# Optimization experiments

Measured on AMD Instinct MI355X. Metric: run time of the kernel, lower is better.

Reference implementation:

```python
import jax, jax.numpy as jnp
import numpy as np

H = 128        # hidden_channels
R = 32         # num_rbf
L = 2          # num_layers
CUTOFF = 4.5   # cutoff_upper (cutoff_lower = 0)
N_ATOMS = 2048
N_EDGES = 32768


def _tensor_norm(t):
    # Frobenius norm squared over the trailing 3x3 -> [N, H]
    return jnp.sum(t * t, axis=(-2, -1))


def _decompose(t):
    # Split into isotropic (I), antisymmetric (A), traceless symmetric (S) parts.
    eye = jnp.eye(3, dtype=t.dtype)
    I = (jnp.trace(t, axis1=-2, axis2=-1) / 3.0)[..., None, None] * eye
    A = 0.5 * (t - jnp.swapaxes(t, -2, -1))
    S = 0.5 * (t + jnp.swapaxes(t, -2, -1)) - I
    return I, A, S


def _chan_mix(T, W):
    # torch nn.Linear(H, H, bias=False) applied on the channel axis of [N,H,3,3]
    return jnp.einsum('nhij,gh->ngij', T, W)


def _interaction(X, edge_index, edge_weight, edge_attr, q,
                 W1, b1, W2, b2, W3, b3, Wt):
    N = X.shape[0]
    src, dst = edge_index[0], edge_index[1]
    # cosine cutoff (cutoff_lower = 0)
    C = 0.5 * (jnp.cos(edge_weight * (jnp.pi / CUTOFF)) + 1.0)
    C = C * (edge_weight < CUTOFF).astype(C.dtype)
    # edge scalar MLP: R -> H -> 2H -> 3H, silu
    ea = jax.nn.silu(edge_attr @ W1.T + b1)
    ea = jax.nn.silu(ea @ W2.T + b2)
    ea = jax.nn.silu(ea @ W3.T + b3)
    ea = (ea * C[:, None]).reshape(-1, H, 3)       # [E, H, 3]
    # normalize node tensors
    X = X / (_tensor_norm(X) + 1.0)[..., None, None]
    I, A, S = _decompose(X)
    I = _chan_mix(I, Wt[0])
    A = _chan_mix(A, Wt[1])
    S = _chan_mix(S, Wt[2])
    Y = I + A + S
    # per-edge tensor messages (Im + Am + Sm fused before the scatter)
    msg = (ea[:, :, 0, None, None] * I[dst]
           + ea[:, :, 1, None, None] * A[dst]
           + ea[:, :, 2, None, None] * S[dst])   # [E, H, 3, 3]
    M = jax.ops.segment_sum(msg, src, num_segments=N)
    # O(3) group: symmetrized tensor product, scaled by charge factor
    AB = jnp.matmul(M, Y) + jnp.matmul(Y, M)
    I, A, S = _decompose((1.0 + 0.1 * q[:, None, None, None]) * AB)
    normp1 = (_tensor_norm(I + A + S) + 1.0)[..., None, None]
    I, A, S = I / normp1, A / normp1, S / normp1
    I = _chan_mix(I, Wt[3])
    A = _chan_mix(A, Wt[4])
    S = _chan_mix(S, Wt[5])
    dX = I + A + S
    return X + dX + (1.0 + 0.1 * q[:, None, None, None]) * jnp.matmul(dX, dX)


def setup_inputs() -> dict:
    key = jax.random.key(0)
    ks = jax.random.split(key, 10)
    N, E = N_ATOMS, N_EDGES
    X = jax.random.normal(ks[0], (N, H, 3, 3), jnp.float32)
    edge_index = jax.random.randint(ks[1], (2, E), 0, N, jnp.int32)
    edge_weight = jax.random.uniform(ks[2], (E,), jnp.float32, 0.1, CUTOFF)
    edge_attr = jax.random.normal(ks[3], (E, R), jnp.float32)
    q = jax.random.normal(ks[4], (N,), jnp.float32) * 0.1
    s = 0.05
    Ws1 = jax.random.normal(ks[5], (L, H, R), jnp.float32) * s
    bs1 = jnp.zeros((L, H), jnp.float32)
    Ws2 = jax.random.normal(ks[6], (L, 2 * H, H), jnp.float32) * s
    bs2 = jnp.zeros((L, 2 * H), jnp.float32)
    Ws3 = jax.random.normal(ks[7], (L, 3 * H, 2 * H), jnp.float32) * s
    bs3 = jnp.zeros((L, 3 * H), jnp.float32)
    Wt = jax.random.normal(ks[8], (L, 6, H, H), jnp.float32) * s
    return dict(X=X, edge_attr=edge_attr, edge_weight=edge_weight, q=q,
                Ws1=Ws1, bs1=bs1, Ws2=Ws2, bs2=bs2, Ws3=Ws3, bs3=bs3,
                Wt=Wt, edge_index=edge_index)


def reference(X, edge_attr, edge_weight, q, Ws1, bs1, Ws2, bs2, Ws3, bs3, Wt, edge_index):
    for l in range(L):
        X = _interaction(X, edge_index, edge_weight, edge_attr, q,
                         Ws1[l], bs1[l], Ws2[l], bs2[l], Ws3[l], bs3[l], Wt[l])
    return X
```

## Files before the change

### kernel.cpp

```cpp
#include <hip/hip_runtime.h>
#include <hip/hip_bf16.h>
#include <math.h>

#define H 128
#define R 32
#define NATOMS 2048
#define NEDGES 32768
#define NH (NATOMS * H)
#define NP 1152
#define CUTOFF_F 4.5f
#define PI_OVER_CUTOFF 0.6981317007977318f

typedef __bf16 bf16x8 __attribute__((ext_vector_type(8)));
typedef float f32x4 __attribute__((ext_vector_type(4)));
typedef short short8 __attribute__((ext_vector_type(8)));
typedef unsigned short u16x4 __attribute__((ext_vector_type(4)));

#define BAR_LGKM() do { \
    asm volatile("s_waitcnt lgkmcnt(0)" ::: "memory"); \
    __builtin_amdgcn_s_barrier(); \
    asm volatile("" ::: "memory"); \
} while (0)

__device__ __forceinline__ float silu_f(float x) {
    return x / (1.f + __expf(-x));
}
__device__ __forceinline__ float b2f(unsigned short u) {
    return __uint_as_float(((unsigned)u) << 16);
}
__device__ __forceinline__ unsigned short f2b(float f) {
    __hip_bfloat16 h = __float2bfloat16(f);
    return __builtin_bit_cast(unsigned short, h);
}

__device__ __forceinline__ void build_full(const float d[9], float m[9]) {
    float i0 = d[0], a01 = d[1], a02 = d[2], a12 = d[3];
    float s00 = d[4], s01 = d[5], s02 = d[6], s11 = d[7], s12 = d[8];
    float s22 = -(s00 + s11);
    m[0] = i0 + s00;  m[1] = a01 + s01;  m[2] = a02 + s02;
    m[3] = s01 - a01; m[4] = i0 + s11;   m[5] = a12 + s12;
    m[6] = s02 - a02; m[7] = s12 - a12;  m[8] = i0 + s22;
}

#define C0 (NEDGES * R)
#define C1 (2 * H * R)
#define C2 (2 * 2 * H * H)
#define C3 (2 * 3 * H * 2 * H)
#define C4 (2 * 6 * H * H)
#define C5 2048
#define CAST_TOTAL (C0 + C1 + C2 + C3 + C4 + C5 + NH)
__global__ __launch_bounds__(256) void k_cast_all(
        const float* __restrict__ ea, const float* __restrict__ w1,
        const float* __restrict__ w2, const float* __restrict__ w3,
        const float* __restrict__ wt,
        __hip_bfloat16* __restrict__ oea, __hip_bfloat16* __restrict__ ow1,
        __hip_bfloat16* __restrict__ ow2, __hip_bfloat16* __restrict__ ow3,
        __hip_bfloat16* __restrict__ owt, int* __restrict__ cnt,
        const float* __restrict__ X, float* __restrict__ Xn,
        __hip_bfloat16* __restrict__ Db) {
    int i = blockIdx.x * 256 + threadIdx.x;
    if (i < C0) { oea[i] = __float2bfloat16(ea[i]); return; }
    i -= C0;
    if (i < C1) { ow1[i] = __float2bfloat16(w1[i]); return; }
    i -= C1;
    if (i < C2) { ow2[i] = __float2bfloat16(w2[i]); return; }
    i -= C2;
    if (i < C3) { ow3[i] = __float2bfloat16(w3[i]); return; }
    i -= C3;
    if (i < C4) { owt[i] = __float2bfloat16(wt[i]); return; }
    i -= C4;
    if (i < C5) { cnt[i] = 0; return; }
    i -= C5;
    if (i < NH) {
        const float* x = X + (size_t)i * 9;
        float v[9];
        float ss = 0.f;
#pragma unroll
        for (int j = 0; j < 9; j++) { v[j] = x[j]; ss += v[j] * v[j]; }
        float inv = 1.f / (ss + 1.f);
#pragma unroll
        for (int j = 0; j < 9; j++) { v[j] *= inv; Xn[(size_t)i * 9 + j] = v[j]; }
        float i0 = (v[0] + v[4] + v[8]) * (1.f / 3.f);
        unsigned short* D = (unsigned short*)Db + (size_t)(i >> 7) * NP + (i & 127);
        D[0 * H] = f2b(i0);
        D[1 * H] = f2b(0.5f * (v[1] - v[3]));
        D[2 * H] = f2b(0.5f * (v[2] - v[6]));
        D[3 * H] = f2b(0.5f * (v[5] - v[7]));
        D[4 * H] = f2b(v[0] - i0);
        D[5 * H] = f2b(0.5f * (v[1] + v[3]));
        D[6 * H] = f2b(0.5f * (v[2] + v[6]));
        D[7 * H] = f2b(v[4] - i0);
        D[8 * H] = f2b(0.5f * (v[5] + v[7]));
    }
}

struct TGm {
    static constexpr int BKm = 64;
    static constexpr int RB  = 128;
    static constexpr int SWZ = 7;
    static constexpr int NIT = 2;
    static constexpr int ABYTES = 128 * RB;
    static constexpr int BBYTES = 64 * RB;
    static constexpr int AISS = ABYTES / 4096;
    static constexpr int BISS = BBYTES / 4096;
    static constexpr int LDSB = ABYTES + BBYTES;
};

__device__ __forceinline__ void tile_gemm_mix(
        const __hip_bfloat16* __restrict__ A, int strideA,
        const __hip_bfloat16* __restrict__ W,
        int m0, int n0, char* lds, f32x4 acc[4][2]) {
    using T = TGm;
    const int t = threadIdx.x;
    const int lane = t & 63;
    const int w = t >> 6;

    auto stage = [&](int b, int it) {
        const int k0 = it * T::BKm;
        char* As = lds + b * T::LDSB;
        char* Bs = As + T::ABYTES;
#pragma unroll
        for (int i = 0; i < T::AISS; i++) {
            int base = (w * T::AISS + i) * 1024;
            int lin = base + lane * 16;
            int row = lin / T::RB;
            int slot = (lin % T::RB) >> 4;
            int sl = slot ^ (row & T::SWZ);
            const char* src = (const char*)(A + (size_t)(m0 + row) * strideA + k0) + sl * 16;
            __builtin_amdgcn_global_load_lds(
                (const __attribute__((address_space(1))) void*)src,
                (__attribute__((address_space(3))) void*)(As + base), 16, 0, 0);
        }
#pragma unroll
        for (int i = 0; i < T::BISS; i++) {
            int base = (w * T::BISS + i) * 1024;
            int lin = base + lane * 16;
            int row = lin / T::RB;
            int slot = (lin % T::RB) >> 4;
            int sl = slot ^ (row & T::SWZ);
            const char* src = (const char*)(W + (size_t)(n0 + row) * H + k0) + sl * 16;
            __builtin_amdgcn_global_load_lds(
                (const __attribute__((address_space(1))) void*)src,
                (__attribute__((address_space(3))) void*)(Bs + base), 16, 0, 0);
        }
    };

    auto compute = [&](int b) {
        const char* As = lds + b * T::LDSB;
        const char* Bs = As + T::ABYTES;
        const int wm = (w & 1) * 64;
        const int wn = (w >> 1) * 32;
        const int rA = wm + (lane & 15);
        const int rB = wn + (lane & 15);
        const int c = lane >> 4;
#pragma unroll
        for (int kk = 0; kk < T::BKm / 32; kk++) {
            bf16x8 av[4], bv[2];
#pragma unroll
            for (int mf = 0; mf < 4; mf++) {
                int row = rA + mf * 16;
                int sp = (kk * 4 + c) ^ (row & T::SWZ);
                av[mf] = __builtin_bit_cast(bf16x8,
                    *(const short8*)(As + row * T::RB + sp * 16));
            }
#pragma unroll
            for (int nf = 0; nf < 2; nf++) {
                int row = rB + nf * 16;
                int sp = (kk * 4 + c) ^ (row & T::SWZ);
                bv[nf] = __builtin_bit_cast(bf16x8,
                    *(const short8*)(Bs + row * T::RB + sp * 16));
            }
#pragma unroll
            for (int mf = 0; mf < 4; mf++)
#pragma unroll
                for (int nf = 0; nf < 2; nf++)
                    acc[mf][nf] = __builtin_amdgcn_mfma_f32_16x16x32_bf16(
                        av[mf], bv[nf], acc[mf][nf], 0, 0, 0);
        }
    };

    stage(0, 0);
    asm volatile("s_waitcnt vmcnt(0)" ::: "memory");
    __syncthreads();
    for (int it = 0; it < T::NIT; it++) {
        int b = it & 1;
        if (it + 1 < T::NIT) stage(b ^ 1, it + 1);
        compute(b);
        asm volatile("s_waitcnt vmcnt(0)" ::: "memory");
        __syncthreads();
    }
}

__global__ __launch_bounds__(256) void k_mix(
        const __hip_bfloat16* __restrict__ Db, const __hip_bfloat16* __restrict__ Wtb,
        __hip_bfloat16* __restrict__ Outp, int partOff) {
    __shared__ char lds[2 * TGm::LDSB];
    int c = blockIdx.z;
    int part = (c == 0) ? 0 : ((c < 4) ? 1 : 2);
    const __hip_bfloat16* A = Db + (size_t)c * H;
    const __hip_bfloat16* W = Wtb + (size_t)(partOff + part) * H * H;
    unsigned short* Out = (unsigned short*)Outp + (size_t)c * H;
    const int lane = threadIdx.x & 63;
    const int w = threadIdx.x >> 6;
    const int wm = (w & 1) * 64, wn = (w >> 1) * 32;
    const int m0 = blockIdx.x * 128, n0 = blockIdx.y * 64;
    f32x4 acc[4][2] = {};
    tile_gemm_mix(A, NP, W, m0, n0, lds, acc);
#pragma unroll
    for (int mf = 0; mf < 4; mf++)
#pragma unroll
        for (int r = 0; r < 4; r++) {
            int row = m0 + wm + mf * 16 + (lane >> 4) * 4 + r;
#pragma unroll
            for (int nf = 0; nf < 2; nf++) {
                int col = n0 + wn + nf * 16 + (lane & 15);
                Out[(size_t)row * NP + col] = f2b(acc[mf][nf][r]);
            }
        }
}

#define ETILE 64
#define PAD0 40
#define PAD1 136
#define PAD2 264
#define SA2_B (ETILE * PAD2 * 2)
#define SA1_B (ETILE * PAD1 * 2)
#define SEA_OFF SA1_B

__global__ __launch_bounds__(512, 4) void k_mlp_fused(
        const __hip_bfloat16* __restrict__ eaB,
        const __hip_bfloat16* __restrict__ W1b, const __hip_bfloat16* __restrict__ W2b,
        const __hip_bfloat16* __restrict__ W3b,
        const float* __restrict__ bs1, const float* __restrict__ bs2,
        const float* __restrict__ bs3, const float* __restrict__ ew,
        __hip_bfloat16* __restrict__ ea3g) {
    const int l = blockIdx.z;
    const unsigned short* W1 = (const unsigned short*)W1b + (size_t)l * (H * R);
    const unsigned short* W2 = (const unsigned short*)W2b + (size_t)l * (2 * H * H);
    const unsigned short* W3 = (const unsigned short*)W3b + (size_t)l * (3 * H * 2 * H);
    const float* b1 = bs1 + (size_t)l * H;
    const float* b2 = bs2 + (size_t)l * 2 * H;
    const float* b3 = bs3 + (size_t)l * 3 * H;
    unsigned short* outp = (unsigned short*)ea3g + (size_t)l * NEDGES * 384;
    const int e0 = blockIdx.x * ETILE;

    __shared__ char smem[SA2_B + ETILE * 4 + 16];
    unsigned short* sA2 = (unsigned short*)smem;
    unsigned short* sA1 = (unsigned short*)smem;
    unsigned short* sEA = (unsigned short*)(smem + SEA_OFF);
    float* sEW = (float*)(smem + SA2_B);

    const int t = threadIdx.x;
    const int lane = t & 63;
    const int w = t >> 6;
    const int q = lane >> 4;
    const int li = lane & 15;

    const int cbase1 = w * 16;
    const int cbase2 = w * 32;
    const int cbase3 = w * 48;

    bf16x8 av1 = __builtin_bit_cast(bf16x8,
        *(const short8*)(W1 + (size_t)(cbase1 + li) * R + q * 8));
    f32x4 bb1 = *(const f32x4*)&b1[cbase1 + q * 4];

    {
        if (t < 256) {
            int row = t >> 2, c8 = t & 3;
            *(uint4*)(sEA + row * PAD0 + c8 * 8) =
                *(const uint4*)((const unsigned short*)eaB + (size_t)(e0 + row) * R + c8 * 8);
        }
        if (t < ETILE) sEW[t] = ew[e0 + t];
    }
    BAR_LGKM();

    f32x4 acc1[4] = {};
#pragma unroll
    for (int ef = 0; ef < 4; ef++) {
        bf16x8 bv = __builtin_bit_cast(bf16x8,
            *(const short8*)(sEA + (ef * 16 + li) * PAD0 + q * 8));
        acc1[ef] = __builtin_amdgcn_mfma_f32_16x16x32_bf16(av1, bv, acc1[ef], 0, 0, 0);
    }

    bf16x8 a2[4][2];
#pragma unroll
    for (int ks = 0; ks < 4; ks++)
#pragma unroll
        for (int mf = 0; mf < 2; mf++)
            a2[ks][mf] = __builtin_bit_cast(bf16x8,
                *(const short8*)(W2 + (size_t)(cbase2 + mf * 16 + li) * H
                                 + ks * 32 + q * 8));
    f32x4 bb2[2];
#pragma unroll
    for (int mf = 0; mf < 2; mf++)
        bb2[mf] = *(const f32x4*)&b2[cbase2 + mf * 16 + q * 4];

#pragma unroll
    for (int ef = 0; ef < 4; ef++) {
        u16x4 o;
#pragma unroll
        for (int r = 0; r < 4; r++) o[r] = f2b(silu_f(acc1[ef][r] + bb1[r]));
        *(u16x4*)(sA1 + (ef * 16 + li) * PAD1 + cbase1 + q * 4) = o;
    }
    BAR_LGKM();

    f32x4 acc2[2][4] = {};
#pragma unroll
    for (int ks = 0; ks < 4; ks++) {
        bf16x8 bv[4];
#pragma unroll
        for (int ef = 0; ef < 4; ef++)
            bv[ef] = __builtin_bit_cast(bf16x8,
                *(const short8*)(sA1 + (ef * 16 + li) * PAD1 + ks * 32 + q * 8));
#pragma unroll
        for (int mf = 0; mf < 2; mf++)
#pragma unroll
            for (int ef = 0; ef < 4; ef++)
                acc2[mf][ef] = __builtin_amdgcn_mfma_f32_16x16x32_bf16(
                    a2[ks][mf], bv[ef], acc2[mf][ef], 0, 0, 0);
    }

    bf16x8 a3[3][3];
#pragma unroll
    for (int pk = 0; pk < 3; pk++)
#pragma unroll
        for (int mf = 0; mf < 3; mf++)
            a3[pk][mf] = __builtin_bit_cast(bf16x8,
                *(const short8*)(W3 + (size_t)(cbase3 + mf * 16 + li) * (2 * H)
                                 + pk * 32 + q * 8));

    BAR_LGKM();
#pragma unroll
    for (int mf = 0; mf < 2; mf++)
#pragma unroll
        for (int ef = 0; ef < 4; ef++) {
            u16x4 o;
#pragma unroll
            for (int r = 0; r < 4; r++)
                o[r] = f2b(silu_f(acc2[mf][ef][r] + bb2[mf][r]));
            *(u16x4*)(sA2 + (ef * 16 + li) * PAD2 + cbase2 + mf * 16 + q * 4) = o;
        }
    BAR_LGKM();

    f32x4 acc3[3][4] = {};
#pragma unroll
    for (int ks = 0; ks < 8; ks++) {
        const int slot = ks % 3;
        bf16x8 bv[4];
#pragma unroll
        for (int ef = 0; ef < 4; ef++)
            bv[ef] = __builtin_bit_cast(bf16x8,
                *(const short8*)(sA2 + (ef * 16 + li) * PAD2 + ks * 32 + q * 8));
#pragma unroll
        for (int mf = 0; mf < 3; mf++)
#pragma unroll
            for (int ef = 0; ef < 4; ef++)
                acc3[mf][ef] = __builtin_amdgcn_mfma_f32_16x16x32_bf16(
                    a3[slot][mf], bv[ef], acc3[mf][ef], 0, 0, 0);
        if (ks + 3 < 8) {
#pragma unroll
            for (int mf = 0; mf < 3; mf++)
                a3[slot][mf] = __builtin_bit_cast(bf16x8,
                    *(const short8*)(W3 + (size_t)(cbase3 + mf * 16 + li) * (2 * H)
                                     + (ks + 3) * 32 + q * 8));
        }
    }
    f32x4 bb3[3];
#pragma unroll
    for (int mf = 0; mf < 3; mf++)
        bb3[mf] = *(const f32x4*)&b3[cbase3 + mf * 16 + q * 4];
#pragma unroll
    for (int ef = 0; ef < 4; ef++) {
        int edge = ef * 16 + li;
        float wv = sEW[edge];
        float cs = (wv < CUTOFF_F) ? 0.5f * (__cosf(wv * PI_OVER_CUTOFF) + 1.f) : 0.f;
#pragma unroll
        for (int mf = 0; mf < 3; mf++) {
            u16x4 o;
#pragma unroll
            for (int r = 0; r < 4; r++)
                o[r] = f2b(silu_f(acc3[mf][ef][r] + bb3[mf][r]) * cs);
            *(u16x4*)(outp + (size_t)(e0 + edge) * 384 + cbase3 + mf * 16 + q * 4) = o;
        }
    }
}

__global__ __launch_bounds__(256) void k_hist(
        const int* __restrict__ eidx, int* __restrict__ cnt) {
    int e = blockIdx.x * 256 + threadIdx.x;
    if (e < NEDGES) atomicAdd(&cnt[eidx[e]], 1);
}

__global__ __launch_bounds__(256) void k_scan(
        const int* __restrict__ cnt, int* __restrict__ rowstart,
        int* __restrict__ cursor) {
    __shared__ int partial[256];
    int t = threadIdx.x;
    int loc[8];
    int run = 0;
#pragma unroll
    for (int j = 0; j < 8; j++) {
        int v = cnt[t * 8 + j];
        loc[j] = run; run += v;
    }
    partial[t] = run;
    __syncthreads();
    if (t == 0) {
        int acc = 0;
        for (int i = 0; i < 256; i++) { int v = partial[i]; partial[i] = acc; acc += v; }
        rowstart[2048] = acc;
    }
    __syncthreads();
    int base = partial[t];
#pragma unroll
    for (int j = 0; j < 8; j++) {
        rowstart[t * 8 + j] = base + loc[j];
        cursor[t * 8 + j] = base + loc[j];
    }
}

__global__ __launch_bounds__(256) void k_fill(
        const int* __restrict__ eidx, int* __restrict__ cursor,
        int* __restrict__ elist) {
    int e = blockIdx.x * 256 + threadIdx.x;
    if (e >= NEDGES) return;
    int src = eidx[e];
    int pos = atomicAdd(&cursor[src], 1);
    elist[pos] = e;
}

__global__ __launch_bounds__(256) void k_gather_ab(
        const __hip_bfloat16* __restrict__ ea ,
        const int* __restrict__ eidx,
        const int* __restrict__ rowstart, const int* __restrict__ elist,
        const __hip_bfloat16* __restrict__ Yb, const float* __restrict__ q,
        __hip_bfloat16* __restrict__ Tb) {
    int gid = blockIdx.x * 256 + threadIdx.x;
    int n = gid >> 7;
    int t7 = gid & 127;
    int hp = t7 >> 1;
    int half = t7 & 1;
    int h0 = hp << 1;
    int beg = rowstart[n], end = rowstart[n + 1];
    const unsigned short* Y = (const unsigned short*)Yb;

    int hcol = h0 + half;
    const unsigned short* ypn = Y + (size_t)n * NP + hcol;
    float yd[9];
#pragma unroll
    for (int c = 0; c < 9; c++) yd[c] = b2f(ypn[(size_t)c * H]);

    float acc[9][2];
#pragma unroll
    for (int c = 0; c < 9; c++) { acc[c][0] = 0.f; acc[c][1] = 0.f; }

    int idx = beg + half;
    int e = 0, dst = 0;
    if (idx < end) { e = elist[idx]; dst = eidx[NEDGES + e]; }
    while (idx < end) {
        int nidx = idx + 2;
        int ne = e, ndst = dst;
        if (nidx < end) { ne = elist[nidx]; ndst = eidx[NEDGES + ne]; }
        const unsigned short* eap = (const unsigned short*)ea + (size_t)e * 384 + h0 * 3;
        unsigned u0 = *(const unsigned*)(eap);
        unsigned u1 = *(const unsigned*)(eap + 2);
        unsigned u2 = *(const unsigned*)(eap + 4);
        float w0a = b2f(u0 & 0xffff), w1a = b2f(u0 >> 16);
        float w2a = b2f(u1 & 0xffff), w0b = b2f(u1 >> 16);
        float w1b = b2f(u2 & 0xffff), w2b = b2f(u2 >> 16);
        const unsigned short* yp = Y + (size_t)dst * NP + h0;
        ushort2 y;
        y = *(const ushort2*)(yp + 0 * H); acc[0][0] += w0a * b2f(y.x); acc[0][1] += w0b * b2f(y.y);
        y = *(const ushort2*)(yp + 1 * H); acc[1][0] += w1a * b2f(y.x); acc[1][1] += w1b * b2f(y.y);
        y = *(const ushort2*)(yp + 2 * H); acc[2][0] += w1a * b2f(y.x); acc[2][1] += w1b * b2f(y.y);
        y = *(const ushort2*)(yp + 3 * H); acc[3][0] += w1a * b2f(y.x); acc[3][1] += w1b * b2f(y.y);
#pragma unroll
        for (int c = 4; c < 9; c++) {
            y = *(const ushort2*)(yp + c * H);
            acc[c][0] += w2a * b2f(y.x); acc[c][1] += w2b * b2f(y.y);
        }
        idx = nidx; e = ne; dst = ndst;
    }
#pragma unroll
    for (int c = 0; c < 9; c++) {
        acc[c][0] += __shfl_xor(acc[c][0], 1);
        acc[c][1] += __shfl_xor(acc[c][1], 1);
    }
    float scale = 1.f + 0.1f * q[n];
    float md[9];
#pragma unroll
    for (int c = 0; c < 9; c++) md[c] = acc[c][half];
    float m[9], yf[9];
    build_full(md, m);
    build_full(yd, yf);
    float ab[9];
#pragma unroll
    for (int ii = 0; ii < 3; ii++)
#pragma unroll
        for (int jj = 0; jj < 3; jj++) {
            float s = 0.f;
#pragma unroll
            for (int kk = 0; kk < 3; kk++)
                s += m[ii * 3 + kk] * yf[kk * 3 + jj] + yf[ii * 3 + kk] * m[kk * 3 + jj];
            ab[ii * 3 + jj] = s;
        }
    float nrm = 0.f;
#pragma unroll
    for (int j = 0; j < 9; j++) { ab[j] *= scale; nrm += ab[j] * ab[j]; }
    float inv = 1.f / (nrm + 1.f);
    float tr3 = (ab[0] + ab[4] + ab[8]) * (1.f / 3.f);
    unsigned short* T = (unsigned short*)Tb + (size_t)n * NP + hcol;
    T[0 * H] = f2b(tr3 * inv);
    T[1 * H] = f2b(0.5f * (ab[1] - ab[3]) * inv);
    T[2 * H] = f2b(0.5f * (ab[2] - ab[6]) * inv);
    T[3 * H] = f2b(0.5f * (ab[5] - ab[7]) * inv);
    T[4 * H] = f2b((ab[0] - tr3) * inv);
    T[5 * H] = f2b(0.5f * (ab[1] + ab[3]) * inv);
    T[6 * H] = f2b(0.5f * (ab[2] + ab[6]) * inv);
    T[7 * H] = f2b((ab[4] - tr3) * inv);
    T[8 * H] = f2b(0.5f * (ab[5] + ab[7]) * inv);
}

template <bool PREP>
__global__ __launch_bounds__(256) void k_final(
        const __hip_bfloat16* __restrict__ dXb, const float* __restrict__ Xn,
        const float* __restrict__ q, float* __restrict__ Xout,
        float* __restrict__ XnW, __hip_bfloat16* __restrict__ Db) {
    int i = blockIdx.x * 256 + threadIdx.x;
    if (i >= NH) return;
    const unsigned short* dX = (const unsigned short*)dXb + (size_t)(i >> 7) * NP + (i & 127);
    float dd[9];
#pragma unroll
    for (int c = 0; c < 9; c++) dd[c] = b2f(dX[(size_t)c * H]);
    float dx[9];
    build_full(dd, dx);
    float scale = 1.f + 0.1f * q[i >> 7];
    float out[9];
#pragma unroll
    for (int ii = 0; ii < 3; ii++)
#pragma unroll
        for (int jj = 0; jj < 3; jj++) {
            float s = 0.f;
#pragma unroll
            for (int kk = 0; kk < 3; kk++)
                s += dx[ii * 3 + kk] * dx[kk * 3 + jj];
            out[ii * 3 + jj] = Xn[(size_t)i * 9 + ii * 3 + jj] + dx[ii * 3 + jj] + scale * s;
        }
#pragma unroll
    for (int j = 0; j < 9; j++) Xout[(size_t)i * 9 + j] = out[j];
    if (PREP) {
        float ss = 0.f;
#pragma unroll
        for (int j = 0; j < 9; j++) ss += out[j] * out[j];
        float inv = 1.f / (ss + 1.f);
        float v[9];
#pragma unroll
        for (int j = 0; j < 9; j++) { v[j] = out[j] * inv; XnW[(size_t)i * 9 + j] = v[j]; }
        float i0 = (v[0] + v[4] + v[8]) * (1.f / 3.f);
        unsigned short* D = (unsigned short*)Db + (size_t)(i >> 7) * NP + (i & 127);
        D[0 * H] = f2b(i0);
        D[1 * H] = f2b(0.5f * (v[1] - v[3]));
        D[2 * H] = f2b(0.5f * (v[2] - v[6]));
        D[3 * H] = f2b(0.5f * (v[5] - v[7]));
        D[4 * H] = f2b(v[0] - i0);
        D[5 * H] = f2b(0.5f * (v[1] + v[3]));
        D[6 * H] = f2b(0.5f * (v[2] + v[6]));
        D[7 * H] = f2b(v[4] - i0);
        D[8 * H] = f2b(0.5f * (v[5] + v[7]));
    }
}

extern "C" void kernel_launch(void* const* d_in, const int* in_sizes, int n_in,
                              void* d_out, int out_size, void* d_ws, size_t ws_size,
                              hipStream_t stream) {
    const float* X          = (const float*)d_in[0];
    const float* edge_attr  = (const float*)d_in[1];
    const float* edge_weight= (const float*)d_in[2];
    const float* q          = (const float*)d_in[3];
    const float* Ws1        = (const float*)d_in[4];
    const float* bs1        = (const float*)d_in[5];
    const float* Ws2        = (const float*)d_in[6];
    const float* bs2        = (const float*)d_in[7];
    const float* Ws3        = (const float*)d_in[8];
    const float* bs3        = (const float*)d_in[9];
    const float* Wt         = (const float*)d_in[10];
    const int*   eidx       = (const int*)d_in[11];
    float* Xout = (float*)d_out;

    char* p = (char*)d_ws;
    auto alloc = [&](size_t bytes) -> char* {
        char* r = p; p += (bytes + 255) & ~(size_t)255; return r;
    };
    size_t nodeBytes = (size_t)NH * 9 * sizeof(float);
    float* Xn   = (float*)alloc(nodeBytes);
    __hip_bfloat16* Db = (__hip_bfloat16*)alloc((size_t)NH * 9 * 2);
    __hip_bfloat16* Yb = (__hip_bfloat16*)alloc((size_t)NH * 9 * 2);
    __hip_bfloat16* eaB = (__hip_bfloat16*)alloc((size_t)C0 * 2);
    __hip_bfloat16* W1b = (__hip_bfloat16*)alloc((size_t)C1 * 2);
    __hip_bfloat16* W2b = (__hip_bfloat16*)alloc((size_t)C2 * 2);
    __hip_bfloat16* W3b = (__hip_bfloat16*)alloc((size_t)C3 * 2);
    __hip_bfloat16* Wtb = (__hip_bfloat16*)alloc((size_t)C4 * 2);
    __hip_bfloat16* ea3g = (__hip_bfloat16*)alloc((size_t)2 * NEDGES * 384 * 2);
    int* cnt      = (int*)alloc(2048 * 4);
    int* rowstart = (int*)alloc(2049 * 4);
    int* cursor   = (int*)alloc(2048 * 4);
    int* elist    = (int*)alloc(NEDGES * 4);

    k_cast_all<<<(CAST_TOTAL + 255) / 256, 256, 0, stream>>>(
        edge_attr, Ws1, Ws2, Ws3, Wt, eaB, W1b, W2b, W3b, Wtb, cnt,
        X, Xn, Db);

    k_hist<<<NEDGES / 256, 256, 0, stream>>>(eidx, cnt);
    k_scan<<<1, 256, 0, stream>>>(cnt, rowstart, cursor);
    k_fill<<<NEDGES / 256, 256, 0, stream>>>(eidx, cursor, elist);

    k_mlp_fused<<<dim3(NEDGES / ETILE, 1, 2), 512, 0, stream>>>(
        eaB, W1b, W2b, W3b, bs1, bs2, bs3, edge_weight, ea3g);

    for (int l = 0; l < 2; l++) {
        const __hip_bfloat16* Wtl = Wtb + (size_t)l * 6 * H * H;
        const __hip_bfloat16* ea3 = ea3g + (size_t)l * NEDGES * 384;

        k_mix<<<dim3(NATOMS / 128, 2, 9), 256, 0, stream>>>(Db, Wtl, Yb, 0);
        k_gather_ab<<<NH / 256, 256, 0, stream>>>(
            ea3, eidx, rowstart, elist, Yb, q, Db);
        k_mix<<<dim3(NATOMS / 128, 2, 9), 256, 0, stream>>>(Db, Wtl, Yb, 3);
        if (l == 0)
            k_final<true><<<NH / 256, 256, 0, stream>>>(Yb, Xn, q, Xout, Xn, Db);
        else
            k_final<false><<<NH / 256, 256, 0, stream>>>(Yb, Xn, q, Xout, nullptr, nullptr);
    }
}
```

Measured before the change: 156.5 us.

## Fuse first-layer channel mix into edge MLP kernel launch; use fast reciprocal

```diff
diff --git a/kernel.cpp b/kernel.cpp
--- a/kernel.cpp
+++ b/kernel.cpp
@@ -22,8 +22,11 @@
     asm volatile("" ::: "memory"); \
 } while (0)
 
+__device__ __forceinline__ float rcp_f(float x) {
+    return __builtin_amdgcn_rcpf(x);
+}
 __device__ __forceinline__ float silu_f(float x) {
-    return x / (1.f + __expf(-x));
+    return x * rcp_f(1.f + __expf(-x));
 }
 __device__ __forceinline__ float b2f(unsigned short u) {
     return __uint_as_float(((unsigned)u) << 16);
@@ -77,7 +80,7 @@
         float ss = 0.f;
 #pragma unroll
         for (int j = 0; j < 9; j++) { v[j] = x[j]; ss += v[j] * v[j]; }
-        float inv = 1.f / (ss + 1.f);
+        float inv = rcp_f(ss + 1.f);
 #pragma unroll
         for (int j = 0; j < 9; j++) { v[j] *= inv; Xn[(size_t)i * 9 + j] = v[j]; }
         float i0 = (v[0] + v[4] + v[8]) * (1.f / 3.f);
@@ -106,10 +109,10 @@
     static constexpr int LDSB = ABYTES + BBYTES;
 };
 
-__device__ __forceinline__ void tile_gemm_mix(
+__device__ __forceinline__ void tile_gemm_mix_g(
         const __hip_bfloat16* __restrict__ A, int strideA,
         const __hip_bfloat16* __restrict__ W,
-        int m0, int n0, char* lds, f32x4 acc[4][2]) {
+        int m0, int n0, char* lds, f32x4 acc[4][2], bool active) {
     using T = TGm;
     const int t = threadIdx.x;
     const int lane = t & 63;
@@ -179,13 +182,13 @@
         }
     };
 
-    stage(0, 0);
+    if (active) stage(0, 0);
     asm volatile("s_waitcnt vmcnt(0)" ::: "memory");
     __syncthreads();
     for (int it = 0; it < T::NIT; it++) {
         int b = it & 1;
-        if (it + 1 < T::NIT) stage(b ^ 1, it + 1);
-        compute(b);
+        if (active && it + 1 < T::NIT) stage(b ^ 1, it + 1);
+        if (active) compute(b);
         asm volatile("s_waitcnt vmcnt(0)" ::: "memory");
         __syncthreads();
     }
@@ -205,7 +208,7 @@
     const int wm = (w & 1) * 64, wn = (w >> 1) * 32;
     const int m0 = blockIdx.x * 128, n0 = blockIdx.y * 64;
     f32x4 acc[4][2] = {};
-    tile_gemm_mix(A, NP, W, m0, n0, lds, acc);
+    tile_gemm_mix_g(A, NP, W, m0, n0, lds, acc, true);
 #pragma unroll
     for (int mf = 0; mf < 4; mf++)
 #pragma unroll
@@ -226,15 +229,54 @@
 #define SA2_B (ETILE * PAD2 * 2)
 #define SA1_B (ETILE * PAD1 * 2)
 #define SEA_OFF SA1_B
-
-__global__ __launch_bounds__(512, 4) void k_mlp_fused(
+#define MIXBLOCKS 288
+#define FAT_LDS (2 * TGm::LDSB + 256)
+
+__global__ __launch_bounds__(512, 3) void k_fat(
         const __hip_bfloat16* __restrict__ eaB,
         const __hip_bfloat16* __restrict__ W1b, const __hip_bfloat16* __restrict__ W2b,
         const __hip_bfloat16* __restrict__ W3b,
         const float* __restrict__ bs1, const float* __restrict__ bs2,
         const float* __restrict__ bs3, const float* __restrict__ ew,
-        __hip_bfloat16* __restrict__ ea3g) {
-    const int l = blockIdx.z;
+        __hip_bfloat16* __restrict__ ea3g,
+        const __hip_bfloat16* __restrict__ Db, const __hip_bfloat16* __restrict__ Wtb,
+        __hip_bfloat16* __restrict__ Yb) {
+    __shared__ char smem[FAT_LDS];
+    int bid = blockIdx.x;
+
+    if (bid < MIXBLOCKS) {
+        int c = bid / 32;
+        int rem = bid & 31;
+        int m0 = (rem & 15) * 128;
+        int n0 = (rem >> 4) * 64;
+        int part = (c == 0) ? 0 : ((c < 4) ? 1 : 2);
+        const __hip_bfloat16* A = Db + (size_t)c * H;
+        const __hip_bfloat16* W = Wtb + (size_t)part * H * H;
+        unsigned short* Out = (unsigned short*)Yb + (size_t)c * H;
+        bool active = threadIdx.x < 256;
+        f32x4 acc[4][2] = {};
+        tile_gemm_mix_g(A, NP, W, m0, n0, smem, acc, active);
+        if (active) {
+            const int lane = threadIdx.x & 63;
+            const int w = threadIdx.x >> 6;
+            const int wm = (w & 1) * 64, wn = (w >> 1) * 32;
+#pragma unroll
+            for (int mf = 0; mf < 4; mf++)
+#pragma unroll
+                for (int r = 0; r < 4; r++) {
+                    int row = m0 + wm + mf * 16 + (lane >> 4) * 4 + r;
+#pragma unroll
+                    for (int nf = 0; nf < 2; nf++) {
+                        int col = n0 + wn + nf * 16 + (lane & 15);
+                        Out[(size_t)row * NP + col] = f2b(acc[mf][nf][r]);
+                    }
+                }
+        }
+        return;
+    }
+    bid -= MIXBLOCKS;
+
+    const int l = bid >> 9;
     const unsigned short* W1 = (const unsigned short*)W1b + (size_t)l * (H * R);
     const unsigned short* W2 = (const unsigned short*)W2b + (size_t)l * (2 * H * H);
     const unsigned short* W3 = (const unsigned short*)W3b + (size_t)l * (3 * H * 2 * H);
@@ -242,9 +284,8 @@
     const float* b2 = bs2 + (size_t)l * 2 * H;
     const float* b3 = bs3 + (size_t)l * 3 * H;
     unsigned short* outp = (unsigned short*)ea3g + (size_t)l * NEDGES * 384;
-    const int e0 = blockIdx.x * ETILE;
-
-    __shared__ char smem[SA2_B + ETILE * 4 + 16];
+    const int e0 = (bid & 511) * ETILE;
+
     unsigned short* sA2 = (unsigned short*)smem;
     unsigned short* sA1 = (unsigned short*)smem;
     unsigned short* sEA = (unsigned short*)(smem + SEA_OFF);
@@ -507,7 +548,7 @@
     float nrm = 0.f;
 #pragma unroll
     for (int j = 0; j < 9; j++) { ab[j] *= scale; nrm += ab[j] * ab[j]; }
-    float inv = 1.f / (nrm + 1.f);
+    float inv = rcp_f(nrm + 1.f);
     float tr3 = (ab[0] + ab[4] + ab[8]) * (1.f / 3.f);
     unsigned short* T = (unsigned short*)Tb + (size_t)n * NP + hcol;
     T[0 * H] = f2b(tr3 * inv);
@@ -552,7 +593,7 @@
         float ss = 0.f;
 #pragma unroll
         for (int j = 0; j < 9; j++) ss += out[j] * out[j];
-        float inv = 1.f / (ss + 1.f);
+        float inv = rcp_f(ss + 1.f);
         float v[9];
 #pragma unroll
         for (int j = 0; j < 9; j++) { v[j] = out[j] * inv; XnW[(size_t)i * 9 + j] = v[j]; }
@@ -614,14 +655,17 @@
     k_scan<<<1, 256, 0, stream>>>(cnt, rowstart, cursor);
     k_fill<<<NEDGES / 256, 256, 0, stream>>>(eidx, cursor, elist);
 
-    k_mlp_fused<<<dim3(NEDGES / ETILE, 1, 2), 512, 0, stream>>>(
-        eaB, W1b, W2b, W3b, bs1, bs2, bs3, edge_weight, ea3g);
+    k_fat<<<MIXBLOCKS + 1024, 512, 0, stream>>>(
+        eaB, W1b, W2b, W3b, bs1, bs2, bs3, edge_weight, ea3g,
+        Db, Wtb, Yb);
 
     for (int l = 0; l < 2; l++) {
         const __hip_bfloat16* Wtl = Wtb + (size_t)l * 6 * H * H;
         const __hip_bfloat16* ea3 = ea3g + (size_t)l * NEDGES * 384;
 
-        k_mix<<<dim3(NATOMS / 128, 2, 9), 256, 0, stream>>>(Db, Wtl, Yb, 0);
+        if (l == 1) {
+            k_mix<<<dim3(NATOMS / 128, 2, 9), 256, 0, stream>>>(Db, Wtl, Yb, 0);
+        }
         k_gather_ab<<<NH / 256, 256, 0, stream>>>(
             ea3, eidx, rowstart, elist, Yb, q, Db);
         k_mix<<<dim3(NATOMS / 128, 2, 9), 256, 0, stream>>>(Db, Wtl, Yb, 3);
```

Measured after the change: 151.5 us. 1.03x faster.
